# Optimization experiments

Hardware: AMD Instinct MI355X
Metric: run time of the kernel (lower is better)

The kernel has to match this reference:

```python
import jax, jax.numpy as jnp
import numpy as np

B, S, P = 256, 1024, 4096   # batch, n_sensors, n_points
NM, H, PD = 64, 128, 128    # n_modes, hidden width, p
C = 1.0                     # speed of light param


def setup_inputs() -> dict:
    key = jax.random.key(0)
    ks = jax.random.split(key, 16)
    w = lambda k, shp: (jax.random.normal(k, shp, jnp.float32) * 0.05)
    return {
        "u0": jax.random.normal(ks[0], (B, S), jnp.float32),
        "x": jax.random.uniform(ks[1], (P,), jnp.float32, -1.0, 1.0),
        "t": jax.random.uniform(ks[2], (P,), jnp.float32, 0.0, 1.0),
        # branch MLP: (2*NM)->128->128->PD
        "bw1": w(ks[3], (H, 2 * NM)), "bb1": jnp.zeros((H,), jnp.float32),
        "bw2": w(ks[4], (H, H)),      "bb2": jnp.zeros((H,), jnp.float32),
        "bw3": w(ks[5], (PD, H)),     "bb3": jnp.zeros((PD,), jnp.float32),
        # trunk MLP: 4->128->128->PD
        "tw1": w(ks[6], (H, 4)),      "tb1": jnp.zeros((H,), jnp.float32),
        "tw2": w(ks[7], (H, H)),      "tb2": jnp.zeros((H,), jnp.float32),
        "tw3": w(ks[8], (PD, H)),     "tb3": jnp.zeros((PD,), jnp.float32),
    }


def _mlp(a, w1, b1, w2, b2, w3, b3):
    a = jax.nn.relu(a @ w1.T + b1)
    a = jax.nn.relu(a @ w2.T + b2)
    return a @ w3.T + b3


def reference(u0, x, t, bw1, bb1, bw2, bb2, bw3, bb3, tw1, tb1, tw2, tb2, tw3, tb3):
    # Fourier coefficients: mean over sensors of u0 * cos/sin(pi*k*xs)
    xs = jnp.linspace(-1.0, 1.0, S, dtype=jnp.float32)          # (S,)
    modes = jnp.arange(1, NM + 1, dtype=jnp.float32)            # (NM,)
    ang = jnp.pi * modes[:, None] * xs[None, :]                 # (NM, S)
    cos_c = (u0 @ jnp.cos(ang).T) / S                           # (B, NM)
    sin_c = (u0 @ jnp.sin(ang).T) / S                           # (B, NM)
    fourier = jnp.concatenate([cos_c, sin_c], axis=1)           # (B, 2*NM)

    branch_out = _mlp(fourier, bw1, bb1, bw2, bb2, bw3, bb3)    # (B, PD)

    xe = jnp.broadcast_to(x[None, :], (u0.shape[0], P))         # (B, P)
    te = jnp.broadcast_to(t[None, :], (u0.shape[0], P))
    pt_sq = te ** 2 - xe ** 2 / (C ** 2)
    # safe sqrt of clamp(pt_sq, min=0)
    proper_time = jnp.sqrt(jnp.where(pt_sq > 0, pt_sq, 0.0) + 0.0)
    causal = (jnp.abs(xe) <= C * te).astype(jnp.float32)
    trunk_feat = jnp.stack([xe, te, proper_time, causal], axis=-1)  # (B, P, 4)

    trunk_out = _mlp(trunk_feat, tw1, tb1, tw2, tb2, tw3, tb3)      # (B, P, PD)

    u_pred = jnp.einsum("bd,bpd->bp", branch_out, trunk_out)        # (B, P)
    return u_pred * causal
```

## Files before the change

kernel.cpp:

```cpp
#include <hip/hip_runtime.h>
#include <hip/hip_fp16.h>
#include <math.h>

#define NMODES 64
#define SDIM   1024
#define BATCH  256
#define PDIM   4096
#define HDIM   128

typedef _Float16 half8 __attribute__((ext_vector_type(8)));
typedef float f32x4 __attribute__((ext_vector_type(4)));

#define WSB_BAST   0
#define WSB_BRANCH (SDIM * HDIM * 4)
#define WSB_T3     (WSB_BRANCH + BATCH * HDIM * 2)

__global__ __launch_bounds__(256) void k_basis_trunk(
    const float* __restrict__ xv, const float* __restrict__ tv,
    const float* __restrict__ tw1, const float* __restrict__ tb1,
    const float* __restrict__ tw2, const float* __restrict__ tb2,
    const float* __restrict__ tw3, const float* __restrict__ tb3,
    float* __restrict__ basT, __half* __restrict__ t3g) {
    __shared__ float h1L[16 * 132];
    __shared__ float h2L[16 * 132];
    __shared__ float featL[16][4];

    const int t = threadIdx.x;

    if (blockIdx.x < 512) {
        int idx = blockIdx.x * 256 + t;
        int s = idx >> 7;
        int j = idx & 127;
        float xs = -1.0f + 2.0f * (float)s / 1023.0f;
        int k = (j & 63) + 1;
        float pk = 3.14159265358979323846f * (float)k;
        float ang = pk * xs;
        basT[idx] = (j < 64) ? cosf(ang) : sinf(ang);
        return;
    }

    const int pbase = (blockIdx.x - 512) * 16;
    const int j = t & 127;
    const int pg = t >> 7;

    if (t < 16) {
        int p = pbase + t;
        float x = xv[p], tt = tv[p];
        float q = tt * tt - x * x;
        float ptime = (q > 0.f) ? sqrtf(q) : 0.f;
        float c = (fabsf(x) <= tt) ? 1.f : 0.f;
        featL[t][0] = x; featL[t][1] = tt; featL[t][2] = ptime; featL[t][3] = c;
    }
    __syncthreads();

    {
        float4 w1 = ((const float4*)tw1)[j];
        float b1 = tb1[j];
        for (int p = pg; p < 16; p += 2) {
            float4 f = *(const float4*)featL[p];
            float v = fmaf(w1.x, f.x, fmaf(w1.y, f.y, fmaf(w1.z, f.z, fmaf(w1.w, f.w, b1))));
            h1L[p * 132 + j] = fmaxf(v, 0.f);
        }
    }
    __syncthreads();

    {
        const float4* wp = (const float4*)(tw2 + (size_t)j * HDIM);
        float bias = tb2[j];
        float acc[8];
#pragma unroll
        for (int q = 0; q < 8; ++q) acc[q] = bias;
        for (int i4 = 0; i4 < 32; ++i4) {
            float4 wv = wp[i4];
#pragma unroll
            for (int q = 0; q < 8; ++q) {
                float4 hv = *(const float4*)&h1L[(pg + q * 2) * 132 + i4 * 4];
                acc[q] += wv.x * hv.x + wv.y * hv.y + wv.z * hv.z + wv.w * hv.w;
            }
        }
#pragma unroll
        for (int q = 0; q < 8; ++q) h2L[(pg + q * 2) * 132 + j] = fmaxf(acc[q], 0.f);
    }
    __syncthreads();

    {
        const float4* wp = (const float4*)(tw3 + (size_t)j * HDIM);
        float bias = tb3[j];
        float acc[8];
#pragma unroll
        for (int q = 0; q < 8; ++q) acc[q] = bias;
        for (int i4 = 0; i4 < 32; ++i4) {
            float4 wv = wp[i4];
#pragma unroll
            for (int q = 0; q < 8; ++q) {
                float4 hv = *(const float4*)&h2L[(pg + q * 2) * 132 + i4 * 4];
                acc[q] += wv.x * hv.x + wv.y * hv.y + wv.z * hv.z + wv.w * hv.w;
            }
        }
#pragma unroll
        for (int q = 0; q < 8; ++q)
            t3g[(size_t)(pbase + pg + q * 2) * HDIM + j] = __float2half(acc[q]);
    }
}

__global__ __launch_bounds__(256) void k_branch(
    const float* __restrict__ u0, const float* __restrict__ basT,
    const float* __restrict__ bw1, const float* __restrict__ bb1,
    const float* __restrict__ bw2, const float* __restrict__ bb2,
    const float* __restrict__ bw3, const float* __restrict__ bb3,
    __half* __restrict__ branch_out) {
    __shared__ float u0s[2][SDIM];
    __shared__ float part[2][2][HDIM];
    __shared__ float fr[2][HDIM];
    __shared__ float hh[2][HDIM];

    const int t = threadIdx.x;
    const int bb = blockIdx.x * 2;
    const int j = t & 127;
    const int half = t >> 7;

    {
        int flat0 = t;
        int row0 = flat0 >> 8, c40 = flat0 & 255;
        ((float4*)u0s[row0])[c40] = ((const float4*)(u0 + (size_t)(bb + row0) * SDIM))[c40];
        int flat1 = t + 256;
        int row1 = flat1 >> 8, c41 = flat1 & 255;
        ((float4*)u0s[row1])[c41] = ((const float4*)(u0 + (size_t)(bb + row1) * SDIM))[c41];
    }
    __syncthreads();

    {
        float a0 = 0.f, a1 = 0.f;
        const float* bp = basT + j;
        const int s_lo = half * 512;
        for (int s0 = s_lo; s0 < s_lo + 512; s0 += 4) {
            float w0 = bp[(s0 + 0) * HDIM];
            float w1 = bp[(s0 + 1) * HDIM];
            float w2 = bp[(s0 + 2) * HDIM];
            float w3 = bp[(s0 + 3) * HDIM];
            float4 ua = *(const float4*)&u0s[0][s0];
            float4 ub = *(const float4*)&u0s[1][s0];
            a0 += w0 * ua.x + w1 * ua.y + w2 * ua.z + w3 * ua.w;
            a1 += w0 * ub.x + w1 * ub.y + w2 * ub.z + w3 * ub.w;
        }
        part[half][0][j] = a0;
        part[half][1][j] = a1;
    }
    __syncthreads();
    if (t < 128) {
        const float sc = 1.0f / (float)SDIM;
        fr[0][j] = (part[0][0][j] + part[1][0][j]) * sc;
        fr[1][j] = (part[0][1][j] + part[1][1][j]) * sc;
    }
    __syncthreads();

    if (t < 128) {
        {
            const float4* wp = (const float4*)(bw1 + (size_t)j * HDIM);
            float c0 = bb1[j], c1 = c0;
            for (int i4 = 0; i4 < 32; ++i4) {
                float4 wv = wp[i4];
                float4 x0 = *(const float4*)&fr[0][i4 * 4];
                float4 x1 = *(const float4*)&fr[1][i4 * 4];
                c0 += wv.x * x0.x + wv.y * x0.y + wv.z * x0.z + wv.w * x0.w;
                c1 += wv.x * x1.x + wv.y * x1.y + wv.z * x1.z + wv.w * x1.w;
            }
            hh[0][j] = fmaxf(c0, 0.f); hh[1][j] = fmaxf(c1, 0.f);
        }
        __syncthreads();
        {
            const float4* wp = (const float4*)(bw2 + (size_t)j * HDIM);
            float c0 = bb2[j], c1 = c0;
            for (int i4 = 0; i4 < 32; ++i4) {
                float4 wv = wp[i4];
                float4 x0 = *(const float4*)&hh[0][i4 * 4];
                float4 x1 = *(const float4*)&hh[1][i4 * 4];
                c0 += wv.x * x0.x + wv.y * x0.y + wv.z * x0.z + wv.w * x0.w;
                c1 += wv.x * x1.x + wv.y * x1.y + wv.z * x1.z + wv.w * x1.w;
            }
            fr[0][j] = fmaxf(c0, 0.f); fr[1][j] = fmaxf(c1, 0.f);
        }
        __syncthreads();
        {
            const float4* wp = (const float4*)(bw3 + (size_t)j * HDIM);
            float c0 = bb3[j], c1 = c0;
            for (int i4 = 0; i4 < 32; ++i4) {
                float4 wv = wp[i4];
                float4 x0 = *(const float4*)&fr[0][i4 * 4];
                float4 x1 = *(const float4*)&fr[1][i4 * 4];
                c0 += wv.x * x0.x + wv.y * x0.y + wv.z * x0.z + wv.w * x0.w;
                c1 += wv.x * x1.x + wv.y * x1.y + wv.z * x1.z + wv.w * x1.w;
            }
            branch_out[(size_t)(bb + 0) * HDIM + j] = __float2half(c0);
            branch_out[(size_t)(bb + 1) * HDIM + j] = __float2half(c1);
        }
    } else {
        __syncthreads();
        __syncthreads();
    }
}

#define LDH 144
__global__ __launch_bounds__(256) void k_final(
    const __half* __restrict__ br_g, const __half* __restrict__ t3g,
    const float* __restrict__ xv, const float* __restrict__ tv,
    float* __restrict__ out) {
    __shared__ _Float16 brL[64 * LDH];
    __shared__ _Float16 ttL[64 * LDH];
    __shared__ float causL[64];

    const int t = threadIdx.x;
    const int rb = blockIdx.x >> 6;
    const int cb = blockIdx.x & 63;

    if (t < 64) {
        int p = cb * 64 + t;
        float x = xv[p], tt = tv[p];
        causL[t] = (fabsf(x) <= tt) ? 1.f : 0.f;
    }

#pragma unroll
    for (int it = 0; it < 4; ++it) {
        int flat = t + 256 * it;
        int row = flat >> 4, c = flat & 15;
        *(float4*)&brL[row * LDH + c * 8] =
            *(const float4*)&br_g[(size_t)(rb * 64 + row) * HDIM + c * 8];
        *(float4*)&ttL[row * LDH + c * 8] =
            *(const float4*)&t3g[(size_t)(cb * 64 + row) * HDIM + c * 8];
    }
    __syncthreads();

    const int lane = t & 63;
    const int w = t >> 6;
    const int lm = lane & 15;
    const int q = lane >> 4;

    f32x4 acc[4] = {f32x4{0,0,0,0}, f32x4{0,0,0,0}, f32x4{0,0,0,0}, f32x4{0,0,0,0}};

    const _Float16* aBase = &brL[(16 * w + lm) * LDH + q * 8];
#pragma unroll
    for (int ks = 0; ks < 4; ++ks) {
        half8 af = *(const half8*)(aBase + ks * 32);
#pragma unroll
        for (int jt = 0; jt < 4; ++jt) {
            half8 bf = *(const half8*)&ttL[(16 * jt + lm) * LDH + q * 8 + ks * 32];
            acc[jt] = __builtin_amdgcn_mfma_f32_16x16x32_f16(af, bf, acc[jt], 0, 0, 0);
        }
    }

#pragma unroll
    for (int jt = 0; jt < 4; ++jt) {
        int col = cb * 64 + 16 * jt + lm;
        float cz = causL[16 * jt + lm];
#pragma unroll
        for (int e = 0; e < 4; ++e) {
            int row = rb * 64 + 16 * w + q * 4 + e;
            out[(size_t)row * PDIM + col] = acc[jt][e] * cz;
        }
    }
}

extern "C" void kernel_launch(void* const* d_in, const int* in_sizes, int n_in,
                              void* d_out, int out_size, void* d_ws, size_t ws_size,
                              hipStream_t stream) {
    const float* u0  = (const float*)d_in[0];
    const float* xv  = (const float*)d_in[1];
    const float* tv  = (const float*)d_in[2];
    const float* bw1 = (const float*)d_in[3];
    const float* bb1 = (const float*)d_in[4];
    const float* bw2 = (const float*)d_in[5];
    const float* bb2 = (const float*)d_in[6];
    const float* bw3 = (const float*)d_in[7];
    const float* bb3 = (const float*)d_in[8];
    const float* tw1 = (const float*)d_in[9];
    const float* tb1 = (const float*)d_in[10];
    const float* tw2 = (const float*)d_in[11];
    const float* tb2 = (const float*)d_in[12];
    const float* tw3 = (const float*)d_in[13];
    const float* tb3 = (const float*)d_in[14];

    char* wsb = (char*)d_ws;
    float*  basT       = (float*)(wsb + WSB_BAST);
    __half* branch_out = (__half*)(wsb + WSB_BRANCH);
    __half* t3g        = (__half*)(wsb + WSB_T3);
    float* out = (float*)d_out;

    hipLaunchKernelGGL(k_basis_trunk, dim3(768), dim3(256), 0, stream,
                       xv, tv, tw1, tb1, tw2, tb2, tw3, tb3, basT, t3g);
    hipLaunchKernelGGL(k_branch, dim3(BATCH / 2), dim3(256), 0, stream,
                       u0, basT, bw1, bb1, bw2, bb2, bw3, bb3, branch_out);
    hipLaunchKernelGGL(k_final, dim3(256), dim3(256), 0, stream,
                       branch_out, t3g, xv, tv, out);
}
```

Measured before the change: 120.4 us.

## Fuse trunk and branch kernels, compute Fourier basis on the fly

```diff
diff --git a/kernel.cpp b/kernel.cpp
--- a/kernel.cpp
+++ b/kernel.cpp
@@ -11,111 +11,96 @@
 typedef _Float16 half8 __attribute__((ext_vector_type(8)));
 typedef float f32x4 __attribute__((ext_vector_type(4)));
 
-#define WSB_BAST   0
-#define WSB_BRANCH (SDIM * HDIM * 4)
-#define WSB_T3     (WSB_BRANCH + BATCH * HDIM * 2)
-
-__global__ __launch_bounds__(256) void k_basis_trunk(
+#define WSB_BRANCH 0
+#define WSB_T3     (BATCH * HDIM * 2)
+
+__global__ __launch_bounds__(256) void k_fused(
+    const float* __restrict__ u0,
     const float* __restrict__ xv, const float* __restrict__ tv,
+    const float* __restrict__ bw1, const float* __restrict__ bb1,
+    const float* __restrict__ bw2, const float* __restrict__ bb2,
+    const float* __restrict__ bw3, const float* __restrict__ bb3,
     const float* __restrict__ tw1, const float* __restrict__ tb1,
     const float* __restrict__ tw2, const float* __restrict__ tb2,
     const float* __restrict__ tw3, const float* __restrict__ tb3,
-    float* __restrict__ basT, __half* __restrict__ t3g) {
+    __half* __restrict__ branch_out, __half* __restrict__ t3g) {
     __shared__ float h1L[16 * 132];
     __shared__ float h2L[16 * 132];
     __shared__ float featL[16][4];
-
-    const int t = threadIdx.x;
-
-    if (blockIdx.x < 512) {
-        int idx = blockIdx.x * 256 + t;
-        int s = idx >> 7;
-        int j = idx & 127;
-        float xs = -1.0f + 2.0f * (float)s / 1023.0f;
-        int k = (j & 63) + 1;
-        float pk = 3.14159265358979323846f * (float)k;
-        float ang = pk * xs;
-        basT[idx] = (j < 64) ? cosf(ang) : sinf(ang);
-        return;
-    }
-
-    const int pbase = (blockIdx.x - 512) * 16;
-    const int j = t & 127;
-    const int pg = t >> 7;
-
-    if (t < 16) {
-        int p = pbase + t;
-        float x = xv[p], tt = tv[p];
-        float q = tt * tt - x * x;
-        float ptime = (q > 0.f) ? sqrtf(q) : 0.f;
-        float c = (fabsf(x) <= tt) ? 1.f : 0.f;
-        featL[t][0] = x; featL[t][1] = tt; featL[t][2] = ptime; featL[t][3] = c;
-    }
-    __syncthreads();
-
-    {
-        float4 w1 = ((const float4*)tw1)[j];
-        float b1 = tb1[j];
-        for (int p = pg; p < 16; p += 2) {
-            float4 f = *(const float4*)featL[p];
-            float v = fmaf(w1.x, f.x, fmaf(w1.y, f.y, fmaf(w1.z, f.z, fmaf(w1.w, f.w, b1))));
-            h1L[p * 132 + j] = fmaxf(v, 0.f);
-        }
-    }
-    __syncthreads();
-
-    {
-        const float4* wp = (const float4*)(tw2 + (size_t)j * HDIM);
-        float bias = tb2[j];
-        float acc[8];
-#pragma unroll
-        for (int q = 0; q < 8; ++q) acc[q] = bias;
-        for (int i4 = 0; i4 < 32; ++i4) {
-            float4 wv = wp[i4];
-#pragma unroll
-            for (int q = 0; q < 8; ++q) {
-                float4 hv = *(const float4*)&h1L[(pg + q * 2) * 132 + i4 * 4];
-                acc[q] += wv.x * hv.x + wv.y * hv.y + wv.z * hv.z + wv.w * hv.w;
-            }
-        }
-#pragma unroll
-        for (int q = 0; q < 8; ++q) h2L[(pg + q * 2) * 132 + j] = fmaxf(acc[q], 0.f);
-    }
-    __syncthreads();
-
-    {
-        const float4* wp = (const float4*)(tw3 + (size_t)j * HDIM);
-        float bias = tb3[j];
-        float acc[8];
-#pragma unroll
-        for (int q = 0; q < 8; ++q) acc[q] = bias;
-        for (int i4 = 0; i4 < 32; ++i4) {
-            float4 wv = wp[i4];
-#pragma unroll
-            for (int q = 0; q < 8; ++q) {
-                float4 hv = *(const float4*)&h2L[(pg + q * 2) * 132 + i4 * 4];
-                acc[q] += wv.x * hv.x + wv.y * hv.y + wv.z * hv.z + wv.w * hv.w;
-            }
-        }
-#pragma unroll
-        for (int q = 0; q < 8; ++q)
-            t3g[(size_t)(pbase + pg + q * 2) * HDIM + j] = __float2half(acc[q]);
-    }
-}
-
-__global__ __launch_bounds__(256) void k_branch(
-    const float* __restrict__ u0, const float* __restrict__ basT,
-    const float* __restrict__ bw1, const float* __restrict__ bb1,
-    const float* __restrict__ bw2, const float* __restrict__ bb2,
-    const float* __restrict__ bw3, const float* __restrict__ bb3,
-    __half* __restrict__ branch_out) {
     __shared__ float u0s[2][SDIM];
     __shared__ float part[2][2][HDIM];
     __shared__ float fr[2][HDIM];
     __shared__ float hh[2][HDIM];
 
     const int t = threadIdx.x;
-    const int bb = blockIdx.x * 2;
+
+    if (blockIdx.x < 256) {
+        const int pbase = blockIdx.x * 16;
+        const int j = t & 127;
+        const int pg = t >> 7;
+
+        if (t < 16) {
+            int p = pbase + t;
+            float x = xv[p], tt = tv[p];
+            float q = tt * tt - x * x;
+            float ptime = (q > 0.f) ? sqrtf(q) : 0.f;
+            float c = (fabsf(x) <= tt) ? 1.f : 0.f;
+            featL[t][0] = x; featL[t][1] = tt; featL[t][2] = ptime; featL[t][3] = c;
+        }
+        __syncthreads();
+
+        {
+            float4 w1 = ((const float4*)tw1)[j];
+            float b1 = tb1[j];
+            for (int p = pg; p < 16; p += 2) {
+                float4 f = *(const float4*)featL[p];
+                float v = fmaf(w1.x, f.x, fmaf(w1.y, f.y, fmaf(w1.z, f.z, fmaf(w1.w, f.w, b1))));
+                h1L[p * 132 + j] = fmaxf(v, 0.f);
+            }
+        }
+        __syncthreads();
+
+        {
+            const float4* wp = (const float4*)(tw2 + (size_t)j * HDIM);
+            float bias = tb2[j];
+            float acc[8];
+#pragma unroll
+            for (int q = 0; q < 8; ++q) acc[q] = bias;
+            for (int i4 = 0; i4 < 32; ++i4) {
+                float4 wv = wp[i4];
+#pragma unroll
+                for (int q = 0; q < 8; ++q) {
+                    float4 hv = *(const float4*)&h1L[(pg + q * 2) * 132 + i4 * 4];
+                    acc[q] += wv.x * hv.x + wv.y * hv.y + wv.z * hv.z + wv.w * hv.w;
+                }
+            }
+#pragma unroll
+            for (int q = 0; q < 8; ++q) h2L[(pg + q * 2) * 132 + j] = fmaxf(acc[q], 0.f);
+        }
+        __syncthreads();
+
+        {
+            const float4* wp = (const float4*)(tw3 + (size_t)j * HDIM);
+            float bias = tb3[j];
+            float acc[8];
+#pragma unroll
+            for (int q = 0; q < 8; ++q) acc[q] = bias;
+            for (int i4 = 0; i4 < 32; ++i4) {
+                float4 wv = wp[i4];
+#pragma unroll
+                for (int q = 0; q < 8; ++q) {
+                    float4 hv = *(const float4*)&h2L[(pg + q * 2) * 132 + i4 * 4];
+                    acc[q] += wv.x * hv.x + wv.y * hv.y + wv.z * hv.z + wv.w * hv.w;
+                }
+            }
+#pragma unroll
+            for (int q = 0; q < 8; ++q)
+                t3g[(size_t)(pbase + pg + q * 2) * HDIM + j] = __float2half(acc[q]);
+        }
+        return;
+    }
+
+    const int bb = (blockIdx.x - 256) * 2;
     const int j = t & 127;
     const int half = t >> 7;
 
@@ -130,18 +115,29 @@
     __syncthreads();
 
     {
+        const int kmode = (j & 63) + 1;
+        const int s_lo = half * 512;
+        float xs0 = -1.0f + 2.0f * (float)s_lo / 1023.0f;
+        float a = 0.5f * (float)kmode * xs0;
+        a = a - floorf(a);
+        const float r = (float)kmode * (1.0f / 1023.0f);
         float a0 = 0.f, a1 = 0.f;
-        const float* bp = basT + j;
-        const int s_lo = half * 512;
-        for (int s0 = s_lo; s0 < s_lo + 512; s0 += 4) {
-            float w0 = bp[(s0 + 0) * HDIM];
-            float w1 = bp[(s0 + 1) * HDIM];
-            float w2 = bp[(s0 + 2) * HDIM];
-            float w3 = bp[(s0 + 3) * HDIM];
-            float4 ua = *(const float4*)&u0s[0][s0];
-            float4 ub = *(const float4*)&u0s[1][s0];
-            a0 += w0 * ua.x + w1 * ua.y + w2 * ua.z + w3 * ua.w;
-            a1 += w0 * ub.x + w1 * ub.y + w2 * ub.z + w3 * ub.w;
+        if (j < 64) {
+#pragma unroll 8
+            for (int s = s_lo; s < s_lo + 512; ++s) {
+                float bas = __builtin_amdgcn_cosf(a);
+                a += r; a = a - floorf(a);
+                a0 += bas * u0s[0][s];
+                a1 += bas * u0s[1][s];
+            }
+        } else {
+#pragma unroll 8
+            for (int s = s_lo; s < s_lo + 512; ++s) {
+                float bas = __builtin_amdgcn_sinf(a);
+                a += r; a = a - floorf(a);
+                a0 += bas * u0s[0][s];
+                a1 += bas * u0s[1][s];
+            }
         }
         part[half][0][j] = a0;
         part[half][1][j] = a1;
@@ -280,15 +276,13 @@
     const float* tb3 = (const float*)d_in[14];
 
     char* wsb = (char*)d_ws;
-    float*  basT       = (float*)(wsb + WSB_BAST);
     __half* branch_out = (__half*)(wsb + WSB_BRANCH);
     __half* t3g        = (__half*)(wsb + WSB_T3);
     float* out = (float*)d_out;
 
-    hipLaunchKernelGGL(k_basis_trunk, dim3(768), dim3(256), 0, stream,
-                       xv, tv, tw1, tb1, tw2, tb2, tw3, tb3, basT, t3g);
-    hipLaunchKernelGGL(k_branch, dim3(BATCH / 2), dim3(256), 0, stream,
-                       u0, basT, bw1, bb1, bw2, bb2, bw3, bb3, branch_out);
+    hipLaunchKernelGGL(k_fused, dim3(384), dim3(256), 0, stream,
+                       u0, xv, tv, bw1, bb1, bw2, bb2, bw3, bb3,
+                       tw1, tb1, tw2, tb2, tw3, tb3, branch_out, t3g);
     hipLaunchKernelGGL(k_final, dim3(256), dim3(256), 0, stream,
                        branch_out, t3g, xv, tv, out);
 }
```

Result: faster. 107.3 us (-10.9%).
